# Kernel optimization log

Measured on AMD Instinct MI355X. Metric: run time of the kernel, lower is better.

## Reference

```python
import jax, jax.numpy as jnp
import numpy as np

NQ, NL, E = 100000, 16384, 1000000
C_IN, C_OUT, D = 128, 4, 3
H = 64        # kernel MLP hidden
PH = 256      # projection hidden


def setup_inputs() -> dict:
    key = jax.random.key(0)
    ks = jax.random.split(key, 16)
    s = 0.05
    return {
        "rndata_flat": jax.random.normal(ks[0], (NL, C_IN), jnp.float32),
        "phys_pos_query": jax.random.uniform(ks[1], (NQ, D), jnp.float32),
        "latent_tokens_pos": jax.random.uniform(ks[2], (NL, D), jnp.float32),
        "edge_index_dst": jax.random.randint(ks[3], (E,), 0, NQ),
        "edge_index_src": jax.random.randint(ks[4], (E,), 0, NL),
        # kernel MLP: (2*D) -> 64 -> 64 -> C_IN, gelu between layers
        "W0": jax.random.normal(ks[5], (2 * D, H), jnp.float32) * s,
        "b0": jnp.zeros((H,), jnp.float32),
        "W1": jax.random.normal(ks[6], (H, H), jnp.float32) * s,
        "b1": jnp.zeros((H,), jnp.float32),
        "W2": jax.random.normal(ks[7], (H, C_IN), jnp.float32) * s,
        "b2": jnp.zeros((C_IN,), jnp.float32),
        # projection ChannelMLP: C_IN -> 256 -> C_OUT, gelu between layers
        "P0": jax.random.normal(ks[8], (C_IN, PH), jnp.float32) * s,
        "pb0": jnp.zeros((PH,), jnp.float32),
        "P1": jax.random.normal(ks[9], (PH, C_OUT), jnp.float32) * s,
        "pb1": jnp.zeros((C_OUT,), jnp.float32),
    }


def reference(rndata_flat, phys_pos_query, latent_tokens_pos,
              edge_index_dst, edge_index_src,
              W0, b0, W1, b1, W2, b2, P0, pb0, P1, pb1):
    nq = phys_pos_query.shape[0]
    # --- IntegralTransform, transform_type='linear', single scale ---
    # gather edge endpoint coordinates: [E, 2*D]
    e_in = jnp.concatenate(
        [phys_pos_query[edge_index_dst], latent_tokens_pos[edge_index_src]], axis=-1)
    # kernel MLP per edge
    h = jax.nn.gelu(e_in @ W0 + b0)
    h = jax.nn.gelu(h @ W1 + b1)
    k = h @ W2 + b2                                   # [E, C_IN]
    # linear transform: kernel * gathered source features
    rep = k * rndata_flat[edge_index_src]             # [E, C_IN]
    # mean aggregation (scatter) over query nodes
    sums = jax.ops.segment_sum(rep, edge_index_dst, num_segments=nq)
    cnt = jax.ops.segment_sum(jnp.ones((rep.shape[0], 1), rep.dtype),
                              edge_index_dst, num_segments=nq)
    agg = sums / jnp.maximum(cnt, 1.0)                # [Nq, C_IN]
    # --- projection ChannelMLP (2 layers) ---
    h2 = jax.nn.gelu(agg @ P0 + pb0)
    return h2 @ P1 + pb1                              # [Nq, C_OUT]
```

## Files before the change

kernel.cpp:

```cpp
#include <hip/hip_runtime.h>


#define BLOCK 256

typedef _Float16 half8 __attribute__((ext_vector_type(8)));
typedef float f32x4 __attribute__((ext_vector_type(4)));


__device__ __forceinline__ float gelu_f(float x) {
    float x3 = x * x * x;
    float t  = 0.7978845608028654f * fmaf(0.044715f, x3, x);
    float e  = __expf(2.0f * t);
    float r  = __builtin_amdgcn_rcpf(e + 1.0f);
    return 0.5f * x * (1.0f + (1.0f - 2.0f * r));
}


__global__ void hist_kernel(const int* __restrict__ dst, int* __restrict__ hist, int E) {
    int e = blockIdx.x * blockDim.x + threadIdx.x;
    if (e < E) atomicAdd(&hist[dst[e]], 1);
}

__global__ __launch_bounds__(1024) void scan_kernel(const int* __restrict__ hist,
                                                    int* __restrict__ start, int n) {
    __shared__ int wsum[16];
    __shared__ int woff[16];
    int tid = threadIdx.x;
    int lane = tid & 63, wid = tid >> 6;
    int carry = 0;
    for (int base = 0; base < n; base += 1024) {
        int i = base + tid;
        int v = (i < n) ? hist[i] : 0;
        int incl = v;
#pragma unroll
        for (int off = 1; off < 64; off <<= 1) {
            int t = __shfl_up(incl, off, 64);
            if (lane >= off) incl += t;
        }
        if (lane == 63) wsum[wid] = incl;
        __syncthreads();
        if (tid == 0) {
            int acc = carry;
#pragma unroll
            for (int w = 0; w < 16; ++w) { woff[w] = acc; acc += wsum[w]; }
            carry = acc;
        }
        __syncthreads();
        if (i < n) start[i] = woff[wid] + incl - v;
        __syncthreads();
    }
    if (threadIdx.x == 0) start[n] = carry;
}

__global__ void scatter_kernel(const int* __restrict__ dst, const int* __restrict__ src,
                               const int* __restrict__ start, int* __restrict__ cursor,
                               int* __restrict__ dsts, int* __restrict__ srcs, int E) {
    int e = blockIdx.x * blockDim.x + threadIdx.x;
    if (e >= E) return;
    int d = dst[e];
    int pos = start[d] + atomicAdd(&cursor[d], 1);
    dsts[pos] = d;
    srcs[pos] = src[e];
}


__global__ void wprep_kernel(const float* __restrict__ W1,
                             const float* __restrict__ W2,
                             char* __restrict__ img) {
    union { _Float16 h[8]; uint4 u; } cv;
    for (int task = threadIdx.x; task < 1536; task += 256) {
        bool isW2 = task >= 512;
        int id = isW2 ? task - 512 : task;
        int n = id >> 3, kc = id & 7;
        const float* W = isW2 ? W2 : W1;
        int N = isW2 ? 128 : 64;
#pragma unroll
        for (int j = 0; j < 8; ++j) cv.h[j] = (_Float16)W[(kc * 8 + j) * N + n];
        *(uint4*)(img + (isW2 ? 8192 : 0) + n * 128 + ((kc ^ (n & 7)) * 16)) = cv.u;
    }
}


template <int QB, bool FUSED_PROJ>
__global__ __launch_bounds__(BLOCK, 3) void fused_kernel(
    const float* __restrict__ rndata,
    const float* __restrict__ qpos,
    const float* __restrict__ lpos,
    const int*   __restrict__ dsts,
    const int*   __restrict__ srcs,
    const int*   __restrict__ start,
    const float* __restrict__ W0, const float* __restrict__ b0,
    const float* __restrict__ b1, const float* __restrict__ b2,
    const uint4* __restrict__ wimg,
    const float* __restrict__ P0, const float* __restrict__ pb0,
    const float* __restrict__ P1, const float* __restrict__ pb1,
    float* __restrict__ agg,
    float* __restrict__ out,
    int nq)
{
    extern __shared__ char smemc[];
    float* sacc = (float*)(smemc + 32768);
    const int tid = threadIdx.x;

    {
        uint4* wdst = (uint4*)(smemc + 8192);
        for (int i = tid; i < 1536; i += BLOCK) wdst[i] = wimg[i];
    }
    for (int i = tid; i < QB * 129; i += BLOCK) sacc[i] = 0.f;

    const int q0   = blockIdx.x * QB;
    const int qend = min(q0 + QB, nq);
    const int e0 = start[q0], e1 = start[qend];
    const int ntiles = (e1 - e0 + 63) >> 6;

    const int m   = tid & 63;
    const int wid = tid >> 6;
    const int wn1 = __builtin_amdgcn_readfirstlane(wid * 16);
    const int col = m & 15;
    const int g   = m >> 4;
    const int arow  = wid * 16 + col;
    const int aoff0 = arow * 128 + (((0 + g) ^ (arow & 7)) * 16);
    const int aoff1 = arow * 128 + (((4 + g) ^ (arow & 7)) * 16);

    float b1v[4], b2v[8];
#pragma unroll
    for (int nt = 0; nt < 4; ++nt) b1v[nt] = b1[nt * 16 + col];
#pragma unroll
    for (int nt = 0; nt < 8; ++nt) b2v[nt] = b2[nt * 16 + col];

    __syncthreads();

    for (int t = 0; t < ntiles; ++t) {
        const int ebase = e0 + (t << 6);
        int  e     = ebase + m;
        bool valid = e < e1;
        int  d = valid ? dsts[e] : q0;
        int  s = valid ? srcs[e] : 0;
        float pin[6];
        {
            const float* pq = qpos + d * 3;
            pin[0] = pq[0]; pin[1] = pq[1]; pin[2] = pq[2];
            const float* pl = lpos + s * 3;
            pin[3] = pl[0]; pin[4] = pl[1]; pin[5] = pl[2];
        }

        float C0[16];
#pragma unroll
        for (int j = 0; j < 16; ++j) C0[j] = b0[wn1 + j];
#pragma unroll
        for (int k = 0; k < 6; ++k) {
            float a = pin[k];
#pragma unroll
            for (int j = 0; j < 16; ++j)
                C0[j] = fmaf(a, W0[k * 64 + wn1 + j], C0[j]);
        }

        __syncthreads();

        {
            union { _Float16 h[8]; uint4 u; } u0, u1;
#pragma unroll
            for (int j = 0; j < 8; ++j) u0.h[j] = (_Float16)gelu_f(C0[j]);
#pragma unroll
            for (int j = 0; j < 8; ++j) u1.h[j] = (_Float16)gelu_f(C0[8 + j]);
            const int c0 = wid * 2;
            *(uint4*)(smemc + m * 128 + (((c0    ) ^ (m & 7)) * 16)) = u0.u;
            *(uint4*)(smemc + m * 128 + (((c0 + 1) ^ (m & 7)) * 16)) = u1.u;
        }
        __syncthreads();

        half8 a0 = *(const half8*)(smemc + aoff0);
        half8 a1 = *(const half8*)(smemc + aoff1);
        f32x4 c1[4];
#pragma unroll
        for (int nt = 0; nt < 4; ++nt) {
            const int  nrow = nt * 16 + col;
            const char* wb  = smemc + 8192 + nrow * 128;
            half8 bb0 = *(const half8*)(wb + (((0 + g) ^ (nrow & 7)) * 16));
            half8 bb1 = *(const half8*)(wb + (((4 + g) ^ (nrow & 7)) * 16));
            f32x4 acc = {b1v[nt], b1v[nt], b1v[nt], b1v[nt]};
            acc = __builtin_amdgcn_mfma_f32_16x16x32_f16(a0, bb0, acc, 0, 0, 0);
            acc = __builtin_amdgcn_mfma_f32_16x16x32_f16(a1, bb1, acc, 0, 0, 0);
            c1[nt] = acc;
        }

#pragma unroll
        for (int nt = 0; nt < 4; ++nt) {
#pragma unroll
            for (int i = 0; i < 4; ++i) {
                const int row = wid * 16 + g * 4 + i;
                const int ch  = nt * 16 + col;
                *(_Float16*)(smemc + row * 128 + (((ch >> 3) ^ (row & 7)) * 16)
                             + (ch & 7) * 2) = (_Float16)gelu_f(c1[nt][i]);
            }
        }

        half8 a2 = *(const half8*)(smemc + aoff0);
        half8 a3 = *(const half8*)(smemc + aoff1);
        f32x4 c2[8];
#pragma unroll
        for (int nt = 0; nt < 8; ++nt) {
            const int  nrow = nt * 16 + col;
            const char* wb  = smemc + 16384 + nrow * 128;
            half8 bb0 = *(const half8*)(wb + (((0 + g) ^ (nrow & 7)) * 16));
            half8 bb1 = *(const half8*)(wb + (((4 + g) ^ (nrow & 7)) * 16));
            f32x4 acc = {b2v[nt], b2v[nt], b2v[nt], b2v[nt]};
            acc = __builtin_amdgcn_mfma_f32_16x16x32_f16(a2, bb0, acc, 0, 0, 0);
            acc = __builtin_amdgcn_mfma_f32_16x16x32_f16(a3, bb1, acc, 0, 0, 0);
            c2[nt] = acc;
        }

#pragma unroll
        for (int i = 0; i < 4; ++i) {
            const int erow = wid * 16 + g * 4 + i;
            const int eidx = ebase + erow;
            if (eidx < e1) {
                const int dd = dsts[eidx];
                const int ss = srcs[eidx];
                const float* rr = rndata + (size_t)ss * 128 + col;
                float*       sr = sacc + (dd - q0) * 129 + col;
#pragma unroll
                for (int nt = 0; nt < 8; ++nt)
                    atomicAdd(&sr[nt * 16], c2[nt][i] * rr[nt * 16]);
            }
        }
    }
    __syncthreads();

    if (!FUSED_PROJ) {
        for (int idx = tid; idx < QB * 128; idx += BLOCK) {
            int ql = idx >> 7, c = idx & 127;
            int q  = q0 + ql;
            if (q < qend) {
                float deg = (float)(start[q + 1] - start[q]);
                agg[(size_t)q * 128 + c] = sacc[ql * 129 + c] / fmaxf(deg, 1.f);
            }
        }
    } else {
        if (tid < QB) {
            int q = q0 + tid;
            if (q < nq) {
                float deg = (float)(start[q + 1] - start[q]);
                float inv = 1.0f / fmaxf(deg, 1.f);
                const float* aq = &sacc[tid * 129];
                float o0 = pb1[0], o1 = pb1[1], o2 = pb1[2], o3 = pb1[3];
#pragma unroll 1
                for (int jj = 0; jj < 256; jj += 8) {
                    float acc[8];
#pragma unroll
                    for (int u = 0; u < 8; ++u) acc[u] = pb0[jj + u];
#pragma unroll
                    for (int i = 0; i < 128; ++i) {
                        float av = aq[i] * inv;
#pragma unroll
                        for (int u = 0; u < 8; ++u)
                            acc[u] = fmaf(av, P0[i * 256 + jj + u], acc[u]);
                    }
#pragma unroll
                    for (int u = 0; u < 8; ++u) {
                        float h = gelu_f(acc[u]);
                        o0 = fmaf(h, P1[(jj + u) * 4 + 0], o0);
                        o1 = fmaf(h, P1[(jj + u) * 4 + 1], o1);
                        o2 = fmaf(h, P1[(jj + u) * 4 + 2], o2);
                        o3 = fmaf(h, P1[(jj + u) * 4 + 3], o3);
                    }
                }
                float4* o4 = (float4*)(out + (size_t)q * 4);
                *o4 = make_float4(o0, o1, o2, o3);
            }
        }
    }
}


__global__ __launch_bounds__(256) void proj_kernel(
    const float* __restrict__ agg,
    const float* __restrict__ P0, const float* __restrict__ pb0,
    const float* __restrict__ P1, const float* __restrict__ pb1,
    float* __restrict__ out, int nq)
{
    int q = blockIdx.x * blockDim.x + threadIdx.x;
    if (q >= nq) return;

    float a[128];
    const float4* ag4 = (const float4*)(agg + (size_t)q * 128);
#pragma unroll
    for (int i = 0; i < 32; ++i) {
        float4 v = ag4[i];
        a[4 * i + 0] = v.x; a[4 * i + 1] = v.y;
        a[4 * i + 2] = v.z; a[4 * i + 3] = v.w;
    }

    float o0 = pb1[0], o1 = pb1[1], o2 = pb1[2], o3 = pb1[3];
#pragma unroll 1
    for (int jj = 0; jj < 256; jj += 8) {
        float acc[8];
#pragma unroll
        for (int u = 0; u < 8; ++u) acc[u] = pb0[jj + u];
#pragma unroll
        for (int i = 0; i < 128; ++i) {
            float av = a[i];
#pragma unroll
            for (int u = 0; u < 8; ++u)
                acc[u] = fmaf(av, P0[i * 256 + jj + u], acc[u]);
        }
#pragma unroll
        for (int u = 0; u < 8; ++u) {
            float h = gelu_f(acc[u]);
            o0 = fmaf(h, P1[(jj + u) * 4 + 0], o0);
            o1 = fmaf(h, P1[(jj + u) * 4 + 1], o1);
            o2 = fmaf(h, P1[(jj + u) * 4 + 2], o2);
            o3 = fmaf(h, P1[(jj + u) * 4 + 3], o3);
        }
    }
    float4* o4 = (float4*)(out + (size_t)q * 4);
    *o4 = make_float4(o0, o1, o2, o3);
}

extern "C" void kernel_launch(void* const* d_in, const int* in_sizes, int n_in,
                              void* d_out, int out_size, void* d_ws, size_t ws_size,
                              hipStream_t stream)
{
    const float* rndata = (const float*)d_in[0];
    const float* qpos   = (const float*)d_in[1];
    const float* lpos   = (const float*)d_in[2];
    const int*   dst    = (const int*)d_in[3];
    const int*   src    = (const int*)d_in[4];
    const float* W0  = (const float*)d_in[5];
    const float* b0  = (const float*)d_in[6];
    const float* W1  = (const float*)d_in[7];
    const float* b1  = (const float*)d_in[8];
    const float* W2  = (const float*)d_in[9];
    const float* b2  = (const float*)d_in[10];
    const float* P0  = (const float*)d_in[11];
    const float* pb0 = (const float*)d_in[12];
    const float* P1  = (const float*)d_in[13];
    const float* pb1 = (const float*)d_in[14];

    int nq = in_sizes[1] / 3;
    int E  = in_sizes[3];

    size_t agg_bytes  = (size_t)nq * 128 * sizeof(float);
    size_t sort_bytes = 0;
    {
        size_t o = 0;
        o += ((size_t)nq * sizeof(int) + 15) & ~(size_t)15;
        o += ((size_t)nq * sizeof(int) + 15) & ~(size_t)15;
        o += ((size_t)(nq + 1) * sizeof(int) + 15) & ~(size_t)15;
        o += ((size_t)E * sizeof(int) + 15) & ~(size_t)15;
        o += ((size_t)E * sizeof(int) + 15) & ~(size_t)15;
        o += 24576;
        sort_bytes = o;
    }
    bool path_a = (agg_bytes + sort_bytes) <= ws_size;

    size_t off = path_a ? agg_bytes : 0;
    auto alloc = [&](size_t bytes) {
        void* p = (char*)d_ws + off;
        off += (bytes + 15) & ~(size_t)15;
        return p;
    };
    float* agg   = (float*)d_ws;
    int* hist    = (int*)alloc((size_t)nq * sizeof(int));
    int* cursor  = (int*)alloc((size_t)nq * sizeof(int));
    int* start   = (int*)alloc((size_t)(nq + 1) * sizeof(int));
    int* dsts    = (int*)alloc((size_t)E * sizeof(int));
    int* srcs    = (int*)alloc((size_t)E * sizeof(int));
    uint4* wimg  = (uint4*)alloc(24576);

    size_t histpad = ((size_t)nq * sizeof(int) + 15) & ~(size_t)15;
    hipMemsetAsync(hist, 0, 2 * histpad, stream);

    wprep_kernel<<<1, 256, 0, stream>>>(W1, W2, (char*)wimg);
    hist_kernel<<<(E + 255) / 256, 256, 0, stream>>>(dst, hist, E);
    scan_kernel<<<1, 1024, 0, stream>>>(hist, start, nq);
    scatter_kernel<<<(E + 255) / 256, 256, 0, stream>>>(dst, src, start, cursor, dsts, srcs, E);

    constexpr int    QB   = 32;
    constexpr size_t SMEM = 32768 + (size_t)QB * 129 * 4;
    int nb = (nq + QB - 1) / QB;

    if (path_a) {
        fused_kernel<QB, false><<<nb, BLOCK, SMEM, stream>>>(
            rndata, qpos, lpos, dsts, srcs, start,
            W0, b0, b1, b2, wimg, P0, pb0, P1, pb1, agg, nullptr, nq);
        proj_kernel<<<(nq + 255) / 256, 256, 0, stream>>>(
            agg, P0, pb0, P1, pb1, (float*)d_out, nq);
    } else {
        fused_kernel<QB, true><<<nb, BLOCK, SMEM, stream>>>(
            rndata, qpos, lpos, dsts, srcs, start,
            W0, b0, b1, b2, wimg, P0, pb0, P1, pb1, nullptr, (float*)d_out, nq);
    }
}
```

Baseline: 1.200 ms.

## Make each wave process independent 16-edge tiles without block barriers

Each wave now owns its own 16-edge tile and a private LDS scratch for the layer-2 activations. The two per-tile __syncthreads are gone, and the first-layer output feeds the MFMA directly from registers in the A-operand layout instead of going through shared memory. Source feature rows are prefetched into registers before the MLP, the query block shrinks from 32 to 12, and launch bounds go to 4 blocks per CU, all to raise occupancy. In exchange, the small tiles waste lanes on low-degree blocks, and the extra live registers (rr 32 floats, b0v) may spill under the tighter launch bound.

```diff
diff --git a/kernel.cpp b/kernel.cpp
--- a/kernel.cpp
+++ b/kernel.cpp
@@ -82,7 +82,7 @@
 
 
 template <int QB, bool FUSED_PROJ>
-__global__ __launch_bounds__(BLOCK, 3) void fused_kernel(
+__global__ __launch_bounds__(BLOCK, 4) void fused_kernel(
     const float* __restrict__ rndata,
     const float* __restrict__ qpos,
     const float* __restrict__ lpos,
@@ -103,7 +103,7 @@
     const int tid = threadIdx.x;
 
     {
-        uint4* wdst = (uint4*)(smemc + 8192);
+        uint4* wdst = (uint4*)smemc;
         for (int i = tid; i < 1536; i += BLOCK) wdst[i] = wimg[i];
     }
     for (int i = tid; i < QB * 129; i += BLOCK) sacc[i] = 0.f;
@@ -111,71 +111,89 @@
     const int q0   = blockIdx.x * QB;
     const int qend = min(q0 + QB, nq);
     const int e0 = start[q0], e1 = start[qend];
-    const int ntiles = (e1 - e0 + 63) >> 6;
+    const int ntl = (e1 - e0 + 15) >> 4;
 
     const int m   = tid & 63;
     const int wid = tid >> 6;
-    const int wn1 = __builtin_amdgcn_readfirstlane(wid * 16);
-    const int col = m & 15;
+    const int c16 = m & 15;
     const int g   = m >> 4;
-    const int arow  = wid * 16 + col;
-    const int aoff0 = arow * 128 + (((0 + g) ^ (arow & 7)) * 16);
-    const int aoff1 = arow * 128 + (((4 + g) ^ (arow & 7)) * 16);
-
+
+    char* hb = smemc + 24576 + wid * 2048;
+    const int aoff0 = c16 * 128 + (((0 + g) ^ (c16 & 7)) * 16);
+    const int aoff1 = c16 * 128 + (((4 + g) ^ (c16 & 7)) * 16);
+
+    float b0v[16];
+#pragma unroll
+    for (int j = 0; j < 8; ++j) { b0v[j] = b0[g * 8 + j]; b0v[8 + j] = b0[32 + g * 8 + j]; }
     float b1v[4], b2v[8];
 #pragma unroll
-    for (int nt = 0; nt < 4; ++nt) b1v[nt] = b1[nt * 16 + col];
-#pragma unroll
-    for (int nt = 0; nt < 8; ++nt) b2v[nt] = b2[nt * 16 + col];
+    for (int nt = 0; nt < 4; ++nt) b1v[nt] = b1[nt * 16 + c16];
+#pragma unroll
+    for (int nt = 0; nt < 8; ++nt) b2v[nt] = b2[nt * 16 + c16];
 
     __syncthreads();
 
-    for (int t = 0; t < ntiles; ++t) {
-        const int ebase = e0 + (t << 6);
-        int  e     = ebase + m;
-        bool valid = e < e1;
-        int  d = valid ? dsts[e] : q0;
-        int  s = valid ? srcs[e] : 0;
+    for (int t = wid; t < ntl; t += 4) {
+        const int eb = e0 + (t << 4);
+
+        const int  eA = eb + c16;
+        const bool vA = eA < e1;
+        const int  dA = vA ? dsts[eA] : q0;
+        const int  sA = vA ? srcs[eA] : 0;
+
+        int d_ep[4], s_ep[4];
+        bool v_ep[4];
+#pragma unroll
+        for (int i = 0; i < 4; ++i) {
+            int ee = eb + g * 4 + i;
+            v_ep[i] = ee < e1;
+            d_ep[i] = v_ep[i] ? dsts[ee] : q0;
+            s_ep[i] = v_ep[i] ? srcs[ee] : 0;
+        }
+
+        float rr[4][8];
+#pragma unroll
+        for (int i = 0; i < 4; ++i) {
+            const float* r = rndata + (size_t)s_ep[i] * 128 + c16;
+#pragma unroll
+            for (int nt = 0; nt < 8; ++nt) rr[i][nt] = r[nt * 16];
+        }
+
         float pin[6];
         {
-            const float* pq = qpos + d * 3;
+            const float* pq = qpos + dA * 3;
             pin[0] = pq[0]; pin[1] = pq[1]; pin[2] = pq[2];
-            const float* pl = lpos + s * 3;
+            const float* pl = lpos + sA * 3;
             pin[3] = pl[0]; pin[4] = pl[1]; pin[5] = pl[2];
         }
 
         float C0[16];
 #pragma unroll
-        for (int j = 0; j < 16; ++j) C0[j] = b0[wn1 + j];
+        for (int j = 0; j < 16; ++j) C0[j] = b0v[j];
 #pragma unroll
         for (int k = 0; k < 6; ++k) {
-            float a = pin[k];
-#pragma unroll
-            for (int j = 0; j < 16; ++j)
-                C0[j] = fmaf(a, W0[k * 64 + wn1 + j], C0[j]);
-        }
-
-        __syncthreads();
-
-        {
-            union { _Float16 h[8]; uint4 u; } u0, u1;
-#pragma unroll
-            for (int j = 0; j < 8; ++j) u0.h[j] = (_Float16)gelu_f(C0[j]);
-#pragma unroll
-            for (int j = 0; j < 8; ++j) u1.h[j] = (_Float16)gelu_f(C0[8 + j]);
-            const int c0 = wid * 2;
-            *(uint4*)(smemc + m * 128 + (((c0    ) ^ (m & 7)) * 16)) = u0.u;
-            *(uint4*)(smemc + m * 128 + (((c0 + 1) ^ (m & 7)) * 16)) = u1.u;
-        }
-        __syncthreads();
-
-        half8 a0 = *(const half8*)(smemc + aoff0);
-        half8 a1 = *(const half8*)(smemc + aoff1);
+            const float a  = pin[k];
+            const float* w = W0 + k * 64 + g * 8;
+            float wv[16];
+            *(float4*)&wv[0]  = *(const float4*)(w);
+            *(float4*)&wv[4]  = *(const float4*)(w + 4);
+            *(float4*)&wv[8]  = *(const float4*)(w + 32);
+            *(float4*)&wv[12] = *(const float4*)(w + 36);
+#pragma unroll
+            for (int j = 0; j < 16; ++j) C0[j] = fmaf(a, wv[j], C0[j]);
+        }
+        union { _Float16 h[8]; half8 v; } u0, u1;
+#pragma unroll
+        for (int j = 0; j < 8; ++j) u0.h[j] = (_Float16)gelu_f(C0[j]);
+#pragma unroll
+        for (int j = 0; j < 8; ++j) u1.h[j] = (_Float16)gelu_f(C0[8 + j]);
+        const half8 a0 = u0.v, a1 = u1.v;
+
         f32x4 c1[4];
 #pragma unroll
         for (int nt = 0; nt < 4; ++nt) {
-            const int  nrow = nt * 16 + col;
-            const char* wb  = smemc + 8192 + nrow * 128;
+            const int  nrow = nt * 16 + c16;
+            const char* wb  = smemc + nrow * 128;
             half8 bb0 = *(const half8*)(wb + (((0 + g) ^ (nrow & 7)) * 16));
             half8 bb1 = *(const half8*)(wb + (((4 + g) ^ (nrow & 7)) * 16));
             f32x4 acc = {b1v[nt], b1v[nt], b1v[nt], b1v[nt]};
@@ -188,20 +206,20 @@
         for (int nt = 0; nt < 4; ++nt) {
 #pragma unroll
             for (int i = 0; i < 4; ++i) {
-                const int row = wid * 16 + g * 4 + i;
-                const int ch  = nt * 16 + col;
-                *(_Float16*)(smemc + row * 128 + (((ch >> 3) ^ (row & 7)) * 16)
-                             + (ch & 7) * 2) = (_Float16)gelu_f(c1[nt][i]);
+                const int row  = g * 4 + i;
+                const int colh = nt * 16 + c16;
+                *(_Float16*)(hb + row * 128 + (((colh >> 3) ^ (row & 7)) * 16)
+                             + (colh & 7) * 2) = (_Float16)gelu_f(c1[nt][i]);
             }
         }
-
-        half8 a2 = *(const half8*)(smemc + aoff0);
-        half8 a3 = *(const half8*)(smemc + aoff1);
+        const half8 a2 = *(const half8*)(hb + aoff0);
+        const half8 a3 = *(const half8*)(hb + aoff1);
+
         f32x4 c2[8];
 #pragma unroll
         for (int nt = 0; nt < 8; ++nt) {
-            const int  nrow = nt * 16 + col;
-            const char* wb  = smemc + 16384 + nrow * 128;
+            const int  nrow = nt * 16 + c16;
+            const char* wb  = smemc + 8192 + nrow * 128;
             half8 bb0 = *(const half8*)(wb + (((0 + g) ^ (nrow & 7)) * 16));
             half8 bb1 = *(const half8*)(wb + (((4 + g) ^ (nrow & 7)) * 16));
             f32x4 acc = {b2v[nt], b2v[nt], b2v[nt], b2v[nt]};
@@ -212,16 +230,11 @@
 
 #pragma unroll
         for (int i = 0; i < 4; ++i) {
-            const int erow = wid * 16 + g * 4 + i;
-            const int eidx = ebase + erow;
-            if (eidx < e1) {
-                const int dd = dsts[eidx];
-                const int ss = srcs[eidx];
-                const float* rr = rndata + (size_t)ss * 128 + col;
-                float*       sr = sacc + (dd - q0) * 129 + col;
+            if (v_ep[i]) {
+                float* sr = sacc + (d_ep[i] - q0) * 129 + c16;
 #pragma unroll
                 for (int nt = 0; nt < 8; ++nt)
-                    atomicAdd(&sr[nt * 16], c2[nt][i] * rr[nt * 16]);
+                    atomicAdd(&sr[nt * 16], c2[nt][i] * rr[i][nt]);
             }
         }
     }
@@ -376,7 +389,7 @@
     scan_kernel<<<1, 1024, 0, stream>>>(hist, start, nq);
     scatter_kernel<<<(E + 255) / 256, 256, 0, stream>>>(dst, src, start, cursor, dsts, srcs, E);
 
-    constexpr int    QB   = 32;
+    constexpr int    QB   = 12;
     constexpr size_t SMEM = 32768 + (size_t)QB * 129 * 4;
     int nb = (nq + QB - 1) / QB;
 
```

Measured after the change: 1.387 ms. +15.6%, slower.
